# Performance work log

Measured on AMD Instinct MI355X. Metric: run time of the kernel, lower is better.

Reference implementation:

```python
import jax, jax.numpy as jnp
import numpy as np

EPS = 1e-5
GROUPS = 32


def conv1x1(x, W, b):
    # x: (B,C,T), W: (O,C), b: (O,)
    return jnp.einsum('bct,oc->bot', x, W) + b[None, :, None]


def group_norm(x, gamma, beta):
    B, C, T = x.shape
    xg = x.reshape(B, GROUPS, (C // GROUPS) * T)
    mu = xg.mean(axis=-1, keepdims=True)
    var = xg.var(axis=-1, keepdims=True)
    xn = ((xg - mu) * jax.lax.rsqrt(var + EPS)).reshape(B, C, T)
    return xn * gamma[None, :, None] + beta[None, :, None]


def block(x, W, b, gamma, beta):
    return jax.nn.relu(group_norm(conv1x1(x, W, b), gamma, beta))


def setup_inputs() -> dict:
    key = jax.random.key(0)
    ks = jax.random.split(key, 8)
    B, C, P, T, TF = 4, 512, 512, 2048, 4096
    inp = {
        'feature': jax.random.normal(ks[0], (B, C, T), jnp.float32),
        'frame_level_feature': jax.random.uniform(ks[1], (B, C, TF), jnp.float32),
        # cur_point_conv: conv1x1 C->P + GN(32,P)
        'W1': jax.random.normal(ks[2], (P, C), jnp.float32) / np.sqrt(C),
        'b1': jnp.zeros((P,), jnp.float32),
        'g1': jnp.ones((P,), jnp.float32),
        'be1': jnp.zeros((P,), jnp.float32),
        # lr_conv: conv1x1 C->2P + GN(32,2P)
        'W2': jax.random.normal(ks[3], (2 * P, C), jnp.float32) / np.sqrt(C),
        'b2': jnp.zeros((2 * P,), jnp.float32),
        'g2': jnp.ones((2 * P,), jnp.float32),
        'be2': jnp.zeros((2 * P,), jnp.float32),
        # proposal_conv: conv1x1 4P->C + GN(32,C)
        'W3': jax.random.normal(ks[4], (C, 4 * P), jnp.float32) / np.sqrt(4 * P),
        'b3': jnp.zeros((C,), jnp.float32),
        'g3': jnp.ones((C,), jnp.float32),
        'be3': jnp.zeros((C,), jnp.float32),
    }
    return inp


def reference(feature, frame_level_feature, W1, b1, g1, be1, W2, b2, g2, be2, W3, b3, g3, be3):
    fm_short = block(feature, W1, b1, g1, be1)          # (B,P,T)
    feat = block(feature, W2, b2, g2, be2)              # (B,2P,T)
    t = feature.shape[2]
    # inverse-CDF resampling (uses batch 0 statistics, as original)
    mean_values = frame_level_feature.mean(axis=1)[0]   # (TF,)
    mean_values = mean_values / mean_values.sum()
    cdf = (jnp.cumsum(mean_values) * t).astype(jnp.int32)
    cdf = jnp.minimum(cdf, t - 1)                       # (TF,)
    # exact vectorization of findNearNum loop: first index with minimal |cdf-i|
    targets = jnp.arange(t, dtype=jnp.int32)
    idx = jnp.argmin(jnp.abs(cdf[None, :] - targets[:, None]), axis=1)  # (t,)
    sampled = frame_level_feature[:, :, idx]            # (B,C,t)
    mixed = jnp.concatenate([sampled, feat, fm_short], axis=1)  # (B,4P,t)
    mixed = block(mixed, W3, b3, g3, be3)               # (B,C,t)
    return (mixed, feat)
```

## Files before the change

kernel.cpp:

```cpp
#include <hip/hip_runtime.h>

typedef unsigned short u16;
typedef unsigned int   u32;
typedef __attribute__((ext_vector_type(8))) short short8;
typedef __attribute__((ext_vector_type(4))) short short4_t;
typedef __attribute__((ext_vector_type(4))) float f32x4;

__device__ __forceinline__ float bf2f(u16 v) {
  return __uint_as_float(((u32)v) << 16);
}
__device__ __forceinline__ u16 f2bf(float f) {
  u32 u = __float_as_uint(f);
  u32 r = (u + 0x7FFFu + ((u >> 16) & 1u)) >> 16;
  return (u16)r;
}
__device__ __forceinline__ float relu(float x) { return x < 0.f ? 0.f : x; }

__device__ __forceinline__ void gld16(const void* g, void* l) {
  __builtin_amdgcn_global_load_lds((const __attribute__((address_space(1))) u32*)g,
                                   (__attribute__((address_space(3))) u32*)l, 16, 0, 0);
}

__global__ void colmean_part_kernel(const float* __restrict__ frame,
                                    double* __restrict__ partD,
                                    float* __restrict__ rawZ) {
  if (blockIdx.x == 0 && blockIdx.y == 0) {
    rawZ[threadIdx.x] = 0.f;
    rawZ[threadIdx.x + 256] = 0.f;
    rawZ[threadIdx.x + 512] = 0.f;
  }
  int tf = blockIdx.x * 256 + threadIdx.x;
  int ch = blockIdx.y;
  const float* f0 = frame + tf + (size_t)ch * 64 * 4096;
  double s = 0.0;
  for (int c = 0; c < 64; ++c) s += (double)f0[(size_t)c * 4096];
  partD[ch * 4096 + tf] = s;
}

__global__ void scanD_kernel(const double* __restrict__ partD, int* __restrict__ cdf) {
  __shared__ double part[256];
  __shared__ double base[256];
  __shared__ double Ss;
  int tid = threadIdx.x;
  double loc[16];
  double s = 0.0;
#pragma unroll
  for (int i = 0; i < 16; ++i) {
    int tf = tid * 16 + i;
    double m = 0.0;
#pragma unroll
    for (int ch = 0; ch < 8; ++ch) m += partD[ch * 4096 + tf];
    loc[i] = m / 512.0;
    s += loc[i];
  }
  part[tid] = s;
  __syncthreads();
  if (tid == 0) {
    double t = 0.0;
    for (int i = 0; i < 256; ++i) t += part[i];
    Ss = t;
  }
  __syncthreads();
  double S = Ss;
  s = 0.0;
#pragma unroll
  for (int i = 0; i < 16; ++i) { loc[i] = loc[i] / S; s += loc[i]; }
  part[tid] = s;
  __syncthreads();
  if (tid == 0) {
    double c = 0.0;
    for (int i = 0; i < 256; ++i) { base[i] = c; c += part[i]; }
  }
  __syncthreads();
  double c = base[tid];
#pragma unroll
  for (int i = 0; i < 16; ++i) {
    c += loc[i];
    int iv = (int)(c * 2048.0);
    cdf[tid * 16 + i] = iv < 2047 ? iv : 2047;
  }
}

__device__ __forceinline__ int lowbound(const int* __restrict__ cdf, int hi0, int v) {
  int lo = 0, hi = hi0;
  while (lo < hi) { int mid = (lo + hi) >> 1; if (cdf[mid] < v) lo = mid + 1; else hi = mid; }
  return lo;
}
__device__ __forceinline__ int argmin_cdf(const int* __restrict__ cdf, int t) {
  int j2 = lowbound(cdf, 4096, t);
  if (j2 == 0) return 0;
  if (j2 == 4096) return lowbound(cdf, 4096, cdf[4095]);
  int d2 = cdf[j2] - t, d1 = t - cdf[j2 - 1];
  if (d2 < d1) return j2;
  return lowbound(cdf, j2, cdf[j2 - 1]);
}

__global__ void gatherTrans_kernel(const float* __restrict__ frame,
                                   const float* __restrict__ feature,
                                   const int* __restrict__ cdf,
                                   const float* __restrict__ W1,
                                   const float* __restrict__ W2,
                                   u16* __restrict__ X3T, u16* __restrict__ featT,
                                   u16* __restrict__ W12b) {
  __shared__ u16 tile[64][65];
  __shared__ int sidx[64];
  int tid = threadIdx.x;
  int zz = blockIdx.z;
  if (zz >= 8) {
    int flat = (zz - 8) * 256 + blockIdx.y * 8 + blockIdx.x;
    int i = (flat * 256 + tid) * 4;
    f32x4 v = *(const f32x4*)(i < 262144 ? W1 + i : W2 + (i - 262144));
    short4_t o;
#pragma unroll
    for (int e = 0; e < 4; ++e) o[e] = (short)f2bf(v[e]);
    *(short4_t*)(W12b + i) = o;
    return;
  }
  int cb = blockIdx.x * 64, t0 = blockIdx.y * 64;
  int b = zz & 3, which = zz >> 2;
  if (which == 0) {
    if (tid < 64) sidx[tid] = argmin_cdf(cdf, t0 + tid);
    __syncthreads();
    const float* fb = frame + (size_t)b * 512 * 4096;
    for (int i = tid; i < 4096; i += 256) {
      int r = i >> 6, tt = i & 63;
      tile[tt][r] = f2bf(fb[(size_t)(cb + r) * 4096 + sidx[tt]]);
    }
    __syncthreads();
    u16* xb = X3T + (size_t)b * 2048 * 2048;
    for (int i = tid; i < 4096; i += 256) {
      int r = i >> 6, cc = i & 63;
      xb[(size_t)(t0 + r) * 2048 + cb + cc] = tile[r][cc];
    }
  } else {
    const float* xb = feature + (size_t)b * 512 * 2048;
    for (int i = tid; i < 4096; i += 256) {
      int r = i >> 6, tt = i & 63;
      tile[tt][r] = f2bf(xb[(size_t)(cb + r) * 2048 + t0 + tt]);
    }
    __syncthreads();
    u16* xtb = featT + (size_t)b * 2048 * 512;
    for (int i = tid; i < 4096; i += 256) {
      int r = i >> 6, cc = i & 63;
      xtb[(size_t)(t0 + r) * 512 + cb + cc] = tile[r][cc];
    }
  }
}

__global__ void convW_kernel(const float* __restrict__ src, u16* __restrict__ dst) {
  int i = (blockIdx.x * 256 + threadIdx.x) * 4;
  f32x4 v = *(const f32x4*)(src + i);
  short4_t o;
#pragma unroll
  for (int e = 0; e < 4; ++e) o[e] = (short)f2bf(v[e]);
  *(short4_t*)(dst + i) = o;
}

__global__ __launch_bounds__(128) void gemm12_kernel(
    const u16* __restrict__ A, const u16* __restrict__ Bt,
    const float* __restrict__ b1, const float* __restrict__ b2,
    float* __restrict__ Y, float* __restrict__ raw1, float* __restrict__ raw2)
{
  const int K = 512;
  __shared__ short As[2][2048];
  __shared__ short Bs[2][4096];
  const int tid = threadIdx.x;
  const int lane = tid & 63;
  const int w = tid >> 6;
  const int nt = blockIdx.x, mt = blockIdx.y, bb = blockIdx.z;
  const u16* Ab = A + (size_t)mt * 64 * K;
  const u16* Bb = Bt + ((size_t)bb * 2048 + (size_t)nt * 128) * K;
  const int lm = lane & 15, lq = lane >> 4;
  f32x4 acc[4][4] = {};

  auto stage = [&](int buf, int kt) {
#pragma unroll
    for (int p = 0; p < 2; ++p) {
      int chunk = tid + 128 * p;
      int row = chunk >> 2;
      int ko = ((chunk & 3) ^ ((row >> 1) & 3)) << 3;
      gld16(Ab + (size_t)row * K + kt + ko, (char*)As[buf] + chunk * 16);
    }
#pragma unroll
    for (int p = 0; p < 4; ++p) {
      int chunk = tid + 128 * p;
      int row = chunk >> 2;
      int ko = ((chunk & 3) ^ ((row >> 1) & 3)) << 3;
      gld16(Bb + (size_t)row * K + kt + ko, (char*)Bs[buf] + chunk * 16);
    }
  };

  stage(0, 0);
  for (int s = 0; s < 16; ++s) {
    int cur = s & 1;
    __syncthreads();
    if (s + 1 < 16) stage(cur ^ 1, (s + 1) << 5);
    short8 af[4], bfv[4];
#pragma unroll
    for (int i = 0; i < 4; ++i) {
      int r = i * 16 + lm;
      af[i] = *(const short8*)(As[cur] + r * 32 + ((lq ^ ((r >> 1) & 3)) << 3));
    }
#pragma unroll
    for (int j = 0; j < 4; ++j) {
      int r = w * 64 + j * 16 + lm;
      bfv[j] = *(const short8*)(Bs[cur] + r * 32 + ((lq ^ ((r >> 1) & 3)) << 3));
    }
#pragma unroll
    for (int i = 0; i < 4; ++i)
#pragma unroll
      for (int j = 0; j < 4; ++j)
        acc[i][j] = __builtin_amdgcn_mfma_f32_16x16x32_bf16(af[i], bfv[j], acc[i][j], 0, 0, 0);
  }

  float s1[4] = {0.f, 0.f, 0.f, 0.f};
  float s2[4] = {0.f, 0.f, 0.f, 0.f};
#pragma unroll
  for (int i = 0; i < 4; ++i) {
    int mbase = mt * 64 + i * 16 + lq * 4;
#pragma unroll
    for (int e = 0; e < 4; ++e) {
      int m = mbase + e;
      float bv = m < 512 ? b1[m] : b2[m - 512];
      float* yp = Y + ((size_t)bb * 1536 + m) * 2048 + nt * 128 + w * 64 + lm;
#pragma unroll
      for (int j = 0; j < 4; ++j) {
        float v = acc[i][j][e] + bv;
        yp[j * 16] = v;
        s1[i] += v; s2[i] += v * v;
      }
    }
  }
#pragma unroll
  for (int i = 0; i < 4; ++i) {
#pragma unroll
    for (int off = 32; off > 0; off >>= 1) {
      s1[i] += __shfl_xor(s1[i], off);
      s2[i] += __shfl_xor(s2[i], off);
    }
  }
  if (lane == 0) {
    if (mt < 8) {
#pragma unroll
      for (int i = 0; i < 4; ++i) {
        int g = mt * 4 + i;
        atomicAdd(&raw1[(bb * 32 + g) * 2],     s1[i]);
        atomicAdd(&raw1[(bb * 32 + g) * 2 + 1], s2[i]);
      }
    } else {
#pragma unroll
      for (int i = 0; i < 2; ++i) {
        int g = (mt - 8) * 2 + i;
        atomicAdd(&raw2[(bb * 32 + g) * 2],     s1[2 * i] + s1[2 * i + 1]);
        atomicAdd(&raw2[(bb * 32 + g) * 2 + 1], s2[2 * i] + s2[2 * i + 1]);
      }
    }
  }
}

__global__ __launch_bounds__(128) void gemm3s_kernel(
    const u16* __restrict__ A, const u16* __restrict__ Bt,
    const float* __restrict__ bias, float* __restrict__ Yp)
{
  const int K = 2048;
  __shared__ short As[2][2048];
  __shared__ short Bs[2][4096];
  const int tid = threadIdx.x;
  const int lane = tid & 63;
  const int w = tid >> 6;
  const int nt = blockIdx.x, mt = blockIdx.y;
  const int bb = blockIdx.z >> 1, ks = blockIdx.z & 1;
  const u16* Ab = A + (size_t)mt * 64 * K + ks * 1024;
  const u16* Bb = Bt + ((size_t)bb * 2048 + (size_t)nt * 128) * K + ks * 1024;
  const int lm = lane & 15, lq = lane >> 4;
  f32x4 acc[4][4] = {};

  auto stage = [&](int buf, int kt) {
#pragma unroll
    for (int p = 0; p < 2; ++p) {
      int chunk = tid + 128 * p;
      int row = chunk >> 2;
      int ko = ((chunk & 3) ^ ((row >> 1) & 3)) << 3;
      gld16(Ab + (size_t)row * K + kt + ko, (char*)As[buf] + chunk * 16);
    }
#pragma unroll
    for (int p = 0; p < 4; ++p) {
      int chunk = tid + 128 * p;
      int row = chunk >> 2;
      int ko = ((chunk & 3) ^ ((row >> 1) & 3)) << 3;
      gld16(Bb + (size_t)row * K + kt + ko, (char*)Bs[buf] + chunk * 16);
    }
  };

  stage(0, 0);
  for (int s = 0; s < 32; ++s) {
    int cur = s & 1;
    __syncthreads();
    if (s + 1 < 32) stage(cur ^ 1, (s + 1) << 5);
    short8 af[4], bfv[4];
#pragma unroll
    for (int i = 0; i < 4; ++i) {
      int r = i * 16 + lm;
      af[i] = *(const short8*)(As[cur] + r * 32 + ((lq ^ ((r >> 1) & 3)) << 3));
    }
#pragma unroll
    for (int j = 0; j < 4; ++j) {
      int r = w * 64 + j * 16 + lm;
      bfv[j] = *(const short8*)(Bs[cur] + r * 32 + ((lq ^ ((r >> 1) & 3)) << 3));
    }
#pragma unroll
    for (int i = 0; i < 4; ++i)
#pragma unroll
      for (int j = 0; j < 4; ++j)
        acc[i][j] = __builtin_amdgcn_mfma_f32_16x16x32_bf16(af[i], bfv[j], acc[i][j], 0, 0, 0);
  }
#pragma unroll
  for (int i = 0; i < 4; ++i) {
    int mbase = mt * 64 + i * 16 + lq * 4;
#pragma unroll
    for (int e = 0; e < 4; ++e) {
      int m = mbase + e;
      float bv = ks ? 0.f : bias[m];
      float* yp = Yp + ((size_t)(ks * 4 + bb) * 512 + m) * 2048 + nt * 128 + w * 64 + lm;
#pragma unroll
      for (int j = 0; j < 4; ++j)
        yp[j * 16] = acc[i][j][e] + bv;
    }
  }
}

__global__ void stats3p_kernel(const float* __restrict__ Yp, float* __restrict__ raw) {
  int chunk = blockIdx.x, g = blockIdx.y, b = blockIdx.z, tid = threadIdx.x;
  const f32x4* base = (const f32x4*)(Yp + ((size_t)b * 512 + g * 16) * 2048
                                        + (size_t)chunk * 4096);
  float s = 0.f, ss = 0.f;
#pragma unroll
  for (int i = 0; i < 4; ++i) {
    f32x4 a = base[tid + 256 * i];
    f32x4 c = base[tid + 256 * i + 1048576];
#pragma unroll
    for (int e = 0; e < 4; ++e) {
      float v = a[e] + c[e];
      s += v; ss += v * v;
    }
  }
  __shared__ float s1[256], s2[256];
  s1[tid] = s; s2[tid] = ss;
  __syncthreads();
  for (int st = 128; st > 0; st >>= 1) {
    if (tid < st) { s1[tid] += s1[tid + st]; s2[tid] += s2[tid + st]; }
    __syncthreads();
  }
  if (tid == 0) {
    atomicAdd(&raw[(b * 32 + g) * 2],     s1[0]);
    atomicAdd(&raw[(b * 32 + g) * 2 + 1], s2[0]);
  }
}

__global__ void normT12_kernel(const float* __restrict__ Y,
                               const float* __restrict__ raw1,
                               const float* __restrict__ raw2,
                               const float* __restrict__ g1, const float* __restrict__ be1,
                               const float* __restrict__ g2, const float* __restrict__ be2,
                               u16* __restrict__ X3T, float* __restrict__ featOut) {
  __shared__ u16 tile[64][65];
  int b = blockIdx.z, t0 = blockIdx.x * 64;
  int yb_idx = blockIdx.y;
  const int gn2 = yb_idx >= 8;
  int c0 = (gn2 ? yb_idx - 8 : yb_idx) * 64;
  const float* raw   = gn2 ? raw2 : raw1;
  const float* gamma = gn2 ? g2 : g1;
  const float* beta  = gn2 ? be2 : be1;
  const float inv_n  = gn2 ? (1.f / 65536.f) : (1.f / 32768.f);
  const int chBase   = gn2 ? 512 : 0;
  const int gShift   = gn2 ? 5 : 4;
  const int colBase  = gn2 ? 512 : 1536;
  const float* yb = Y + ((size_t)b * 1536 + chBase) * 2048;
  for (int i = threadIdx.x; i < 4096; i += 256) {
    int r = i >> 6, cc = i & 63;
    int ch = c0 + r;
    int gI = (b * 32 + (ch >> gShift)) * 2;
    float mu = raw[gI] * inv_n;
    float var = raw[gI + 1] * inv_n - mu * mu;
    float rs = 1.0f / sqrtf(var + 1e-5f);
    float v = yb[(size_t)ch * 2048 + t0 + cc];
    float o = relu((v - mu) * rs * gamma[ch] + beta[ch]);
    tile[cc][r] = f2bf(o);
    if (gn2) featOut[((size_t)b * 1024 + ch) * 2048 + t0 + cc] = o;
  }
  __syncthreads();
  for (int i = threadIdx.x; i < 4096; i += 256) {
    int r = i >> 6, cc = i & 63;
    X3T[((size_t)b * 2048 + t0 + r) * 2048 + colBase + c0 + cc] = tile[r][cc];
  }
}

__global__ void norm3_kernel(const float* __restrict__ Yp, const float* __restrict__ raw,
                             const float* __restrict__ gamma, const float* __restrict__ beta,
                             float* __restrict__ out) {
  int i4 = blockIdx.x * 256 + threadIdx.x;
  int b = i4 >> 18;
  int ch = (i4 >> 9) & 511;
  int gI = (b * 32 + (ch >> 4)) * 2;
  float mu = raw[gI] * (1.f / 32768.f);
  float var = raw[gI + 1] * (1.f / 32768.f) - mu * mu;
  float rs = 1.0f / sqrtf(var + 1e-5f);
  float ga = gamma[ch], bt = beta[ch];
  f32x4 a = ((const f32x4*)Yp)[i4];
  f32x4 c = ((const f32x4*)Yp)[i4 + 1048576];
  f32x4 o;
#pragma unroll
  for (int e = 0; e < 4; ++e)
    o[e] = relu((a[e] + c[e] - mu) * rs * ga + bt);
  ((f32x4*)out)[i4] = o;
}

extern "C" void kernel_launch(void* const* d_in, const int* in_sizes, int n_in,
                              void* d_out, int out_size, void* d_ws, size_t ws_size,
                              hipStream_t stream) {
  const float* feature = (const float*)d_in[0];
  const float* frame   = (const float*)d_in[1];
  const float* W1 = (const float*)d_in[2];
  const float* b1 = (const float*)d_in[3];
  const float* g1 = (const float*)d_in[4];
  const float* be1 = (const float*)d_in[5];
  const float* W2 = (const float*)d_in[6];
  const float* b2 = (const float*)d_in[7];
  const float* g2 = (const float*)d_in[8];
  const float* be2 = (const float*)d_in[9];
  const float* W3 = (const float*)d_in[10];
  const float* b3 = (const float*)d_in[11];
  const float* g3 = (const float*)d_in[12];
  const float* be3 = (const float*)d_in[13];

  char* ws = (char*)d_ws;
  u16*    X3T   = (u16*)(ws + 0);
  float*  Y12f  = (float*)(ws + 33554432);
  float*  Y3p   = (float*)(ws + 33554432);
  u16*    W3b   = (u16*)(ws + 67108864);
  double* partD = (double*)(ws + 50331648);
  u16*    featT = (u16*)(ws + 83886080);
  u16*    W12b  = (u16*)(ws + 92274688);
  int*    cdf   = (int*)(ws + 93847552);
  float*  raw1  = (float*)(ws + 93872128);
  float*  raw2  = (float*)(ws + 93873152);
  float*  raw3  = (float*)(ws + 93874176);

  float* outMixed = (float*)d_out;
  float* outFeat  = outMixed + (size_t)4 * 512 * 2048;

  colmean_part_kernel<<<dim3(16, 8), 256, 0, stream>>>(frame, partD, raw1);
  scanD_kernel<<<1, 256, 0, stream>>>(partD, cdf);
  gatherTrans_kernel<<<dim3(8, 32, 11), 256, 0, stream>>>(frame, feature, cdf,
                                                          W1, W2, X3T, featT, W12b);
  gemm12_kernel<<<dim3(16, 24, 4), 128, 0, stream>>>(W12b, featT, b1, b2, Y12f,
                                                     raw1, raw2);
  normT12_kernel<<<dim3(32, 24, 4), 256, 0, stream>>>(Y12f, raw1, raw2,
                                                      g1, be1, g2, be2,
                                                      X3T, outFeat);
  convW_kernel<<<1024, 256, 0, stream>>>(W3, W3b);
  gemm3s_kernel<<<dim3(16, 8, 8), 128, 0, stream>>>(W3b, X3T, b3, Y3p);
  stats3p_kernel<<<dim3(8, 32, 4), 256, 0, stream>>>(Y3p, raw3);
  norm3_kernel<<<4096, 256, 0, stream>>>(Y3p, raw3, g3, be3, outMixed);
}
```

Before: 258.4 us.

## Fuse GN3 stats and normalize into one per-group kernel; fold W3 conversion

```diff
diff --git a/kernel.cpp b/kernel.cpp
--- a/kernel.cpp
+++ b/kernel.cpp
@@ -27,7 +27,6 @@
   if (blockIdx.x == 0 && blockIdx.y == 0) {
     rawZ[threadIdx.x] = 0.f;
     rawZ[threadIdx.x + 256] = 0.f;
-    rawZ[threadIdx.x + 512] = 0.f;
   }
   int tf = blockIdx.x * 256 + threadIdx.x;
   int ch = blockIdx.y;
@@ -147,15 +146,6 @@
   }
 }
 
-__global__ void convW_kernel(const float* __restrict__ src, u16* __restrict__ dst) {
-  int i = (blockIdx.x * 256 + threadIdx.x) * 4;
-  f32x4 v = *(const f32x4*)(src + i);
-  short4_t o;
-#pragma unroll
-  for (int e = 0; e < 4; ++e) o[e] = (short)f2bf(v[e]);
-  *(short4_t*)(dst + i) = o;
-}
-
 __global__ __launch_bounds__(128) void gemm12_kernel(
     const u16* __restrict__ A, const u16* __restrict__ Bt,
     const float* __restrict__ b1, const float* __restrict__ b2,
@@ -329,43 +319,29 @@
   }
 }
 
-__global__ void stats3p_kernel(const float* __restrict__ Yp, float* __restrict__ raw) {
-  int chunk = blockIdx.x, g = blockIdx.y, b = blockIdx.z, tid = threadIdx.x;
-  const f32x4* base = (const f32x4*)(Yp + ((size_t)b * 512 + g * 16) * 2048
-                                        + (size_t)chunk * 4096);
-  float s = 0.f, ss = 0.f;
-#pragma unroll
-  for (int i = 0; i < 4; ++i) {
-    f32x4 a = base[tid + 256 * i];
-    f32x4 c = base[tid + 256 * i + 1048576];
-#pragma unroll
-    for (int e = 0; e < 4; ++e) {
-      float v = a[e] + c[e];
-      s += v; ss += v * v;
-    }
-  }
-  __shared__ float s1[256], s2[256];
-  s1[tid] = s; s2[tid] = ss;
-  __syncthreads();
-  for (int st = 128; st > 0; st >>= 1) {
-    if (tid < st) { s1[tid] += s1[tid + st]; s2[tid] += s2[tid + st]; }
-    __syncthreads();
-  }
-  if (tid == 0) {
-    atomicAdd(&raw[(b * 32 + g) * 2],     s1[0]);
-    atomicAdd(&raw[(b * 32 + g) * 2 + 1], s2[0]);
-  }
-}
-
 __global__ void normT12_kernel(const float* __restrict__ Y,
                                const float* __restrict__ raw1,
                                const float* __restrict__ raw2,
                                const float* __restrict__ g1, const float* __restrict__ be1,
                                const float* __restrict__ g2, const float* __restrict__ be2,
+                               const float* __restrict__ W3, u16* __restrict__ W3b,
                                u16* __restrict__ X3T, float* __restrict__ featOut) {
   __shared__ u16 tile[64][65];
   int b = blockIdx.z, t0 = blockIdx.x * 64;
   int yb_idx = blockIdx.y;
+  if (yb_idx == 24) {
+    int flat = blockIdx.z * 32 + blockIdx.x;
+#pragma unroll
+    for (int k = 0; k < 8; ++k) {
+      int i = (flat * 2048 + k * 256 + threadIdx.x) * 4;
+      f32x4 v = *(const f32x4*)(W3 + i);
+      short4_t o;
+#pragma unroll
+      for (int e = 0; e < 4; ++e) o[e] = (short)f2bf(v[e]);
+      *(short4_t*)(W3b + i) = o;
+    }
+    return;
+  }
   const int gn2 = yb_idx >= 8;
   int c0 = (gn2 ? yb_idx - 8 : yb_idx) * 64;
   const float* raw   = gn2 ? raw2 : raw1;
@@ -395,24 +371,60 @@
   }
 }
 
-__global__ void norm3_kernel(const float* __restrict__ Yp, const float* __restrict__ raw,
-                             const float* __restrict__ gamma, const float* __restrict__ beta,
-                             float* __restrict__ out) {
-  int i4 = blockIdx.x * 256 + threadIdx.x;
-  int b = i4 >> 18;
-  int ch = (i4 >> 9) & 511;
-  int gI = (b * 32 + (ch >> 4)) * 2;
-  float mu = raw[gI] * (1.f / 32768.f);
-  float var = raw[gI + 1] * (1.f / 32768.f) - mu * mu;
-  float rs = 1.0f / sqrtf(var + 1e-5f);
-  float ga = gamma[ch], bt = beta[ch];
-  f32x4 a = ((const f32x4*)Yp)[i4];
-  f32x4 c = ((const f32x4*)Yp)[i4 + 1048576];
-  f32x4 o;
-#pragma unroll
-  for (int e = 0; e < 4; ++e)
-    o[e] = relu((a[e] + c[e] - mu) * rs * ga + bt);
-  ((f32x4*)out)[i4] = o;
+__global__ __launch_bounds__(1024) void norm3g_kernel(
+    const float* __restrict__ Yp,
+    const float* __restrict__ gamma, const float* __restrict__ beta,
+    float* __restrict__ out)
+{
+  const int tid = threadIdx.x;
+  const int g = blockIdx.x;
+  const int b = blockIdx.y;
+  const f32x4* a4 = (const f32x4*)(Yp + ((size_t)b * 512 + g * 16) * 2048);
+  const f32x4* c4 = a4 + 1048576;
+  f32x4 v[8];
+  float s = 0.f, ss = 0.f;
+#pragma unroll
+  for (int k = 0; k < 8; ++k) {
+    int f = tid + k * 1024;
+    f32x4 a = a4[f], c = c4[f];
+#pragma unroll
+    for (int e = 0; e < 4; ++e) {
+      float x = a[e] + c[e];
+      v[k][e] = x;
+      s += x; ss += x * x;
+    }
+  }
+#pragma unroll
+  for (int off = 32; off > 0; off >>= 1) {
+    s  += __shfl_xor(s, off);
+    ss += __shfl_xor(ss, off);
+  }
+  __shared__ float w1[16], w2[16];
+  __shared__ float stat[2];
+  int wave = tid >> 6, lane = tid & 63;
+  if (lane == 0) { w1[wave] = s; w2[wave] = ss; }
+  __syncthreads();
+  if (tid == 0) {
+    float t1 = 0.f, t2 = 0.f;
+    for (int i = 0; i < 16; ++i) { t1 += w1[i]; t2 += w2[i]; }
+    float mu = t1 * (1.f / 32768.f);
+    stat[0] = mu;
+    stat[1] = 1.0f / sqrtf(t2 * (1.f / 32768.f) - mu * mu + 1e-5f);
+  }
+  __syncthreads();
+  const float mu = stat[0], rs = stat[1];
+  f32x4* o4 = (f32x4*)(out + ((size_t)b * 512 + g * 16) * 2048);
+#pragma unroll
+  for (int k = 0; k < 8; ++k) {
+    int f = tid + k * 1024;
+    int ch = g * 16 + (f >> 9);
+    float ga = gamma[ch], bt = beta[ch];
+    f32x4 o;
+#pragma unroll
+    for (int e = 0; e < 4; ++e)
+      o[e] = relu((v[k][e] - mu) * rs * ga + bt);
+    o4[f] = o;
+  }
 }
 
 extern "C" void kernel_launch(void* const* d_in, const int* in_sizes, int n_in,
@@ -437,14 +449,13 @@
   u16*    X3T   = (u16*)(ws + 0);
   float*  Y12f  = (float*)(ws + 33554432);
   float*  Y3p   = (float*)(ws + 33554432);
-  u16*    W3b   = (u16*)(ws + 67108864);
   double* partD = (double*)(ws + 50331648);
   u16*    featT = (u16*)(ws + 83886080);
+  u16*    W3b   = (u16*)(ws + 83886080);
   u16*    W12b  = (u16*)(ws + 92274688);
   int*    cdf   = (int*)(ws + 93847552);
   float*  raw1  = (float*)(ws + 93872128);
   float*  raw2  = (float*)(ws + 93873152);
-  float*  raw3  = (float*)(ws + 93874176);
 
   float* outMixed = (float*)d_out;
   float* outFeat  = outMixed + (size_t)4 * 512 * 2048;
@@ -455,11 +466,9 @@
                                                           W1, W2, X3T, featT, W12b);
   gemm12_kernel<<<dim3(16, 24, 4), 128, 0, stream>>>(W12b, featT, b1, b2, Y12f,
                                                      raw1, raw2);
-  normT12_kernel<<<dim3(32, 24, 4), 256, 0, stream>>>(Y12f, raw1, raw2,
+  normT12_kernel<<<dim3(32, 25, 4), 256, 0, stream>>>(Y12f, raw1, raw2,
                                                       g1, be1, g2, be2,
-                                                      X3T, outFeat);
-  convW_kernel<<<1024, 256, 0, stream>>>(W3, W3b);
+                                                      W3, W3b, X3T, outFeat);
   gemm3s_kernel<<<dim3(16, 8, 8), 128, 0, stream>>>(W3b, X3T, b3, Y3p);
-  stats3p_kernel<<<dim3(8, 32, 4), 256, 0, stream>>>(Y3p, raw3);
-  norm3_kernel<<<4096, 256, 0, stream>>>(Y3p, raw3, g3, be3, outMixed);
-}
+  norm3g_kernel<<<dim3(32, 4), 1024, 0, stream>>>(Y3p, g3, be3, outMixed);
+}
```

Result: no change. 258.0 us (-0.1%).
